# Optimization experiments

Hardware: AMD Instinct MI355X
Metric: run time of the kernel (lower is better)

Reference implementation:

```python
import jax, jax.numpy as jnp
import numpy as np

B, T, D = 1, 2048, 1024
HQ, HKV, HD = 16, 4, 64
G = HQ // HKV
E, TOPK, F = 8, 2, 2752
LB = 0.01
SCALE = HD ** -0.5


def setup_inputs() -> dict:
    key = jax.random.key(0)
    ks = jax.random.split(key, 12)
    s = 0.02
    return {
        "x": jax.random.normal(ks[0], (B, T, D), jnp.float32),
        "g1": jnp.ones((D,), jnp.float32),
        "g2": jnp.ones((D,), jnp.float32),
        "wq": jax.random.normal(ks[1], (D, HQ * HD), jnp.float32) * s,
        "wk": jax.random.normal(ks[2], (D, HKV * HD), jnp.float32) * s,
        "wv": jax.random.normal(ks[3], (D, HKV * HD), jnp.float32) * s,
        "wo": jax.random.normal(ks[4], (D, D), jnp.float32) * s,
        "gate_w": jax.random.normal(ks[5], (D, E), jnp.float32) * s,
        "we_gate": jax.random.normal(ks[6], (E, D, F), jnp.float32) * s,
        "we_up": jax.random.normal(ks[7], (E, D, F), jnp.float32) * s,
        "we_down": jax.random.normal(ks[8], (E, F, D), jnp.float32) * s,
    }


def _rmsnorm(x, g, eps=1e-6):
    return x * g * jax.lax.rsqrt(jnp.mean(x * x, axis=-1, keepdims=True) + eps)


def _rope(q, k):
    # q: [B,HQ,T,HD], k: [B,HKV,T,HD]; standard rotate-half RoPE
    pos = jnp.arange(T, dtype=jnp.float32)
    inv_freq = 1.0 / (10000.0 ** (jnp.arange(0, HD, 2, dtype=jnp.float32) / HD))
    ang = pos[:, None] * inv_freq[None, :]                  # [T, HD/2]
    cos = jnp.concatenate([jnp.cos(ang), jnp.cos(ang)], -1)  # [T, HD]
    sin = jnp.concatenate([jnp.sin(ang), jnp.sin(ang)], -1)

    def rot_half(x):
        x1, x2 = jnp.split(x, 2, axis=-1)
        return jnp.concatenate([-x2, x1], axis=-1)

    def apply(x):
        return x * cos + rot_half(x) * sin
    return apply(q), apply(k)


def _attention(x, g1, wq, wk, wv, wo):
    h = _rmsnorm(x, g1)
    q = (h @ wq).reshape(B, T, HQ, HD).transpose(0, 2, 1, 3)   # [B,HQ,T,HD]
    k = (h @ wk).reshape(B, T, HKV, HD).transpose(0, 2, 1, 3)  # [B,HKV,T,HD]
    v = (h @ wv).reshape(B, T, HKV, HD).transpose(0, 2, 1, 3)
    q, k = _rope(q, k)
    qg = q.reshape(B, HKV, G, T, HD)
    # grouped scores without materializing repeated K/V
    scores = jnp.einsum('bkgtd,bksd->bkgts', qg, k) * SCALE     # [B,HKV,G,T,T]
    causal = jnp.tril(jnp.ones((T, T), bool))
    scores = jnp.where(causal, scores, jnp.float32(-jnp.inf))
    w = jax.nn.softmax(scores, axis=-1)
    o = jnp.einsum('bkgts,bksd->bkgtd', w, v)                  # [B,HKV,G,T,HD]
    o = o.reshape(B, HQ, T, HD).transpose(0, 2, 1, 3).reshape(B, T, D)
    return o @ wo


def _moe(x, g2, gate_w, we_gate, we_up, we_down):
    h = _rmsnorm(x, g2).reshape(B * T, D)                      # [N,D]
    N = B * T
    logits = h @ gate_w                                        # [N,E]
    probs = jax.nn.softmax(logits, axis=-1)
    topv, topi = jax.lax.top_k(probs, TOPK)                    # [N,TOPK]
    topv = topv / (topv.sum(-1, keepdims=True) + 1e-8)
    # dense combine weights [N,E]: same math as masked per-expert dispatch
    combine = jnp.zeros((N, E), h.dtype).at[jnp.arange(N)[:, None], topi].add(topv)
    gh = jnp.einsum('nd,edf->enf', h, we_gate)
    up = jnp.einsum('nd,edf->enf', h, we_up)
    y = jnp.einsum('enf,efd->end', jax.nn.silu(gh) * up, we_down)
    out = jnp.einsum('end,ne->nd', y, combine).reshape(B, T, D)
    # load-balancing aux loss
    frac = jnp.zeros((E,), probs.dtype).at[topi.reshape(-1)].add(1.0) / (N * TOPK)
    load = probs.mean(axis=0)
    aux = LB * E * jnp.sum(frac * load)
    return out, aux


def reference(x, g1, g2, wq, wk, wv, wo, gate_w, we_gate, we_up, we_down):
    x = x + _attention(x, g1, wq, wk, wv, wo)
    moe_out, aux = _moe(x, g2, gate_w, we_gate, we_up, we_down)
    x = x + moe_out
    return x, aux
```

## Files before the change

### kernel.cpp

```cpp
#include <hip/hip_runtime.h>
#include <cstdint>

typedef __attribute__((ext_vector_type(8))) short short8;
typedef __attribute__((ext_vector_type(4))) float floatx4;
typedef __attribute__((ext_vector_type(4))) unsigned short ushort4v;
typedef unsigned short ushort;

#define T_LEN 2048
#define D_DIM 1024
#define HQn 16
#define HKVn 4
#define NE 8
#define FF 2752
#define NTOK 2048
#define NSLOT 4096
#define ATT_SCALE 0.125f
#define GATE_TPB 16

#define WAITCNT(N) asm volatile("s_waitcnt vmcnt(" #N ")" ::: "memory")

__device__ inline ushort f2bf(float f) {
  union { float f; unsigned int i; } v; v.f = f;
  unsigned int r = v.i + 0x7fffu + ((v.i >> 16) & 1u);
  return (ushort)(r >> 16);
}
__device__ inline float bf2f(ushort h) {
  union { unsigned int i; float f; } v; v.i = ((unsigned int)h) << 16;
  return v.f;
}
__device__ inline void split8(const float* v, short8& hi, short8& lo) {
#pragma unroll
  for (int i = 0; i < 8; i++) {
    ushort h = f2bf(v[i]);
    hi[i] = (short)h;
    lo[i] = (short)f2bf(v[i] - bf2f(h));
  }
}
__device__ inline floatx4 mfma16(short8 a, short8 b, floatx4 c) {
  return __builtin_amdgcn_mfma_f32_16x16x32_bf16(a, b, c, 0, 0, 0);
}
#define DMA16(g, l)                                                              \
  __builtin_amdgcn_global_load_lds((const __attribute__((address_space(1))) void*)(g), \
                                   (__attribute__((address_space(3))) void*)(l), 16, 0, 0)

__global__ __launch_bounds__(256) void k_cvtT(const float* __restrict__ src,
                                              ushort* __restrict__ dst, int R, int C) {
  __shared__ float tile[32][33];
  size_t sb = (size_t)blockIdx.z * R * C;
  const float* s = src + sb;
  ushort* d = dst + sb;
  int r0 = blockIdx.y * 32, c0 = blockIdx.x * 32;
  int tc = threadIdx.x & 31, tr = threadIdx.x >> 5;
#pragma unroll
  for (int i = 0; i < 4; i++)
    tile[tr + i * 8][tc] = s[(size_t)(r0 + tr + i * 8) * C + c0 + tc];
  __syncthreads();
#pragma unroll
  for (int i = 0; i < 4; i++) {
    int cc = tr + i * 8;
    d[(size_t)(c0 + cc) * R + r0 + tc] = f2bf(tile[tc][cc]);
  }
}

__global__ __launch_bounds__(256) void k_cvtT2(const float* __restrict__ src,
                                               ushort* __restrict__ dh,
                                               ushort* __restrict__ dl, int R, int C) {
  __shared__ float tile[32][33];
  int r0 = blockIdx.y * 32, c0 = blockIdx.x * 32;
  int tc = threadIdx.x & 31, tr = threadIdx.x >> 5;
#pragma unroll
  for (int i = 0; i < 4; i++)
    tile[tr + i * 8][tc] = src[(size_t)(r0 + tr + i * 8) * C + c0 + tc];
  __syncthreads();
#pragma unroll
  for (int i = 0; i < 4; i++) {
    int cc = tr + i * 8;
    float v = tile[tc][cc];
    ushort h = f2bf(v);
    dh[(size_t)(c0 + cc) * R + r0 + tc] = h;
    dl[(size_t)(c0 + cc) * R + r0 + tc] = f2bf(v - bf2f(h));
  }
}

__global__ __launch_bounds__(256) void k_rmsnorm2(const float* __restrict__ x,
                                                  const float* __restrict__ g,
                                                  ushort* __restrict__ oh,
                                                  ushort* __restrict__ ol) {
  int row = blockIdx.x;
  int t = threadIdx.x;
  const float4* x4 = (const float4*)(x + (size_t)row * D_DIM);
  float4 v = x4[t];
  float ss = v.x * v.x + v.y * v.y + v.z * v.z + v.w * v.w;
#pragma unroll
  for (int off = 32; off; off >>= 1) ss += __shfl_xor(ss, off, 64);
  __shared__ float red[4];
  if ((t & 63) == 0) red[t >> 6] = ss;
  __syncthreads();
  float tot = red[0] + red[1] + red[2] + red[3];
  float sc = rsqrtf(tot * (1.0f / D_DIM) + 1e-6f);
  const float4* g4 = (const float4*)g;
  float4 gv = g4[t];
  float vals[4] = {v.x * gv.x * sc, v.y * gv.y * sc, v.z * gv.z * sc, v.w * gv.w * sc};
  ushort4v h4, l4;
#pragma unroll
  for (int i = 0; i < 4; i++) {
    ushort h = f2bf(vals[i]);
    h4[i] = h;
    l4[i] = f2bf(vals[i] - bf2f(h));
  }
  *(ushort4v*)(oh + (size_t)row * D_DIM + t * 4) = h4;
  *(ushort4v*)(ol + (size_t)row * D_DIM + t * 4) = l4;
}

__global__ __launch_bounds__(256) void k_sgemm(const ushort* __restrict__ Ahg,
                                               const ushort* __restrict__ Alg,
                                               const ushort* __restrict__ Bhg,
                                               const ushort* __restrict__ Blg,
                                               float* __restrict__ C,
                                               const float* __restrict__ res,
                                               int N, int K) {
  __shared__ __align__(16) ushort L[36864];
  int tid = threadIdx.x;
  int m0 = blockIdx.y * 64, n0 = blockIdx.x * 128;
  int wave = tid >> 6, lane = tid & 63, quad = lane >> 4, l15 = lane & 15;
  int wm = (wave >> 1) * 32, wn = (wave & 1) * 64;
  floatx4 acc[2][4];
#pragma unroll
  for (int i = 0; i < 2; i++)
#pragma unroll
    for (int j = 0; j < 4; j++) acc[i][j] = (floatx4){0.f, 0.f, 0.f, 0.f};
  const ushort* src[6];
  int off[6];
  int srow = lane >> 2;
  int kc = ((lane & 3) ^ ((lane >> 3) & 3)) * 8;
#pragma unroll
  for (int j = 0; j < 6; j++) {
    int c = wave * 6 + j;
    if (c < 4) {
      src[j] = Ahg + (size_t)(m0 + c * 16 + srow) * K + kc;
      off[j] = c * 512;
    } else if (c < 8) {
      src[j] = Alg + (size_t)(m0 + (c - 4) * 16 + srow) * K + kc;
      off[j] = 2048 + (c - 4) * 512;
    } else if (c < 16) {
      src[j] = Bhg + (size_t)(n0 + (c - 8) * 16 + srow) * K + kc;
      off[j] = 4096 + (c - 8) * 512;
    } else {
      src[j] = Blg + (size_t)(n0 + (c - 16) * 16 + srow) * K + kc;
      off[j] = 8192 + (c - 16) * 512;
    }
  }
  auto stage = [&](ushort* Ld, int k0) {
#pragma unroll
    for (int j = 0; j < 6; j++) DMA16(src[j] + k0, Ld + off[j]);
  };
  auto compute = [&](const ushort* Ld) {
    const ushort* Ah = Ld;
    const ushort* Al = Ld + 2048;
    const ushort* Bh = Ld + 4096;
    const ushort* Bl = Ld + 8192;
    short8 ah[2], al[2], bh[4], bl[4];
#pragma unroll
    for (int mt = 0; mt < 2; mt++) {
      int ar = wm + mt * 16 + l15;
      int sw = (quad ^ ((ar >> 1) & 3)) * 8;
      ah[mt] = *(short8*)&Ah[ar * 32 + sw];
      al[mt] = *(short8*)&Al[ar * 32 + sw];
    }
#pragma unroll
    for (int nt = 0; nt < 4; nt++) {
      int br = wn + nt * 16 + l15;
      int sw = (quad ^ ((br >> 1) & 3)) * 8;
      bh[nt] = *(short8*)&Bh[br * 32 + sw];
      bl[nt] = *(short8*)&Bl[br * 32 + sw];
    }
#pragma unroll
    for (int mt = 0; mt < 2; mt++)
#pragma unroll
      for (int nt = 0; nt < 4; nt++) {
        acc[mt][nt] = mfma16(ah[mt], bh[nt], acc[mt][nt]);
        acc[mt][nt] = mfma16(ah[mt], bl[nt], acc[mt][nt]);
        acc[mt][nt] = mfma16(al[mt], bh[nt], acc[mt][nt]);
      }
  };
  int ntile = K >> 5;
  stage(L, 0);
  stage(L + 12288, 32);
  int cb = 0;
  for (int t = 0; t < ntile; t++) {
    if (t + 1 < ntile) { WAITCNT(6); } else { WAITCNT(0); }
    __builtin_amdgcn_s_barrier();
    __builtin_amdgcn_sched_barrier(0);
    if (t + 2 < ntile) {
      int sb = cb + 2; if (sb >= 3) sb -= 3;
      stage(L + sb * 12288, (t + 2) << 5);
    }
    compute(L + cb * 12288);
    if (++cb == 3) cb = 0;
  }
#pragma unroll
  for (int mt = 0; mt < 2; mt++) {
    int row = m0 + wm + mt * 16 + quad * 4;
#pragma unroll
    for (int nt2 = 0; nt2 < 4; nt2++) {
      int col = n0 + wn + nt2 * 16 + l15;
#pragma unroll
      for (int r = 0; r < 4; r++) {
        float v = acc[mt][nt2][r];
        if (res) v += res[(size_t)(row + r) * N + col];
        C[(size_t)(row + r) * N + col] = v;
      }
    }
  }
}

__global__ __launch_bounds__(256) void k_rope_cvt(const float* __restrict__ qkvf,
                                                  ushort* __restrict__ qhi,
                                                  ushort* __restrict__ qlo,
                                                  ushort* __restrict__ khi,
                                                  ushort* __restrict__ klo) {
  int t = blockIdx.x;
  const float* row = qkvf + (size_t)t * 1536;
  for (int it = threadIdx.x; it < (HQn + HKVn) * 32; it += 256) {
    int hh = it >> 5, i = it & 31;
    float inv = powf(10000.0f, -(float)i / 32.0f);
    float ang = (float)t * inv;
    float c = cosf(ang), s = sinf(ang);
    const float* p;
    ushort *dh, *dl;
    size_t base;
    if (hh < HQn) {
      p = row + hh * 64;
      base = ((size_t)hh * T_LEN + t) * 64;
      dh = qhi; dl = qlo;
    } else {
      int h2 = hh - HQn;
      p = row + 1024 + h2 * 64;
      base = ((size_t)h2 * T_LEN + t) * 64;
      dh = khi; dl = klo;
    }
    float a = p[i], b = p[i + 32];
    float v0 = a * c - b * s;
    float v1 = b * c + a * s;
    ushort h0 = f2bf(v0);
    dh[base + i] = h0;
    dl[base + i] = f2bf(v0 - bf2f(h0));
    ushort h1 = f2bf(v1);
    dh[base + i + 32] = h1;
    dl[base + i + 32] = f2bf(v1 - bf2f(h1));
  }
}

__global__ __launch_bounds__(256) void k_vT(const float* __restrict__ qkvf,
                                            ushort* __restrict__ vbth,
                                            ushort* __restrict__ vbtl) {
  __shared__ float tile[32][33];
  int t0 = blockIdx.x * 32;
  int dh = blockIdx.y;
  int col0 = 1280 + dh * 32;
  int tc = threadIdx.x & 31, tr = threadIdx.x >> 5;
#pragma unroll
  for (int i = 0; i < 4; i++)
    tile[tr + i * 8][tc] = qkvf[(size_t)(t0 + tr + i * 8) * 1536 + col0 + tc];
  __syncthreads();
#pragma unroll
  for (int i = 0; i < 4; i++) {
    int dd = tr + i * 8;
    float v = tile[tc][dd];
    ushort h = f2bf(v);
    size_t idx = (size_t)(dh * 32 + dd) * T_LEN + t0 + tc;
    vbth[idx] = h;
    vbtl[idx] = f2bf(v - bf2f(h));
  }
}

__global__ __launch_bounds__(256) void k_attn(const ushort* __restrict__ qhi,
                                              const ushort* __restrict__ qlo,
                                              const ushort* __restrict__ khi,
                                              const ushort* __restrict__ klo,
                                              const ushort* __restrict__ vbth,
                                              const ushort* __restrict__ vbtl,
                                              ushort* __restrict__ obh,
                                              ushort* __restrict__ obl) {
  __shared__ __align__(16) ushort Kh[4096], Kl[4096], Vh[4096], Vl[4096];
  __shared__ ushort Psh[4 * 16 * 72], Psl[4 * 16 * 72];
  int qh = blockIdx.y, kvh = qh >> 2;
  int tid = threadIdx.x, wave = tid >> 6, lane = tid & 63;
  int quad = lane >> 4, l15 = lane & 15;
  int sx = l15 >> 1;
  int rlb = lane >> 3;
  int csb = (lane & 7) ^ (lane >> 4);
#pragma unroll 1
  for (int hf = 0; hf < 2; hf++) {
    int xt = hf ? (31 - (int)blockIdx.x) : (int)blockIdx.x;
    int r0 = xt * 64;
    const ushort* qbh_ = qhi + ((size_t)qh * T_LEN + r0 + wave * 16 + l15) * 64;
    const ushort* qbl_ = qlo + ((size_t)qh * T_LEN + r0 + wave * 16 + l15) * 64;
    short8 aqh0 = *(const short8*)&qbh_[quad * 8];
    short8 aqh1 = *(const short8*)&qbh_[32 + quad * 8];
    short8 aql0 = *(const short8*)&qbl_[quad * 8];
    short8 aql1 = *(const short8*)&qbl_[32 + quad * 8];
    floatx4 oacc[4];
#pragma unroll
    for (int nt = 0; nt < 4; nt++) oacc[nt] = (floatx4){0.f, 0.f, 0.f, 0.f};
    float mrun[4], lrun[4];
#pragma unroll
    for (int r = 0; r < 4; r++) { mrun[r] = -INFINITY; lrun[r] = 0.f; }
    for (int cc = 0; cc <= xt; cc++) {
      __syncthreads();
      if (wave < 2) {
        const ushort* G = (wave == 0) ? khi : klo;
        ushort* L = (wave == 0) ? Kh : Kl;
        size_t rbase = (size_t)kvh * T_LEN + cc * 64;
#pragma unroll
        for (int i = 0; i < 8; i++) {
          int ch = csb ^ ((i & 1) * 4);
          DMA16(G + (rbase + i * 8 + rlb) * 64 + ch * 8, L + i * 512);
        }
      } else {
        const ushort* G = (wave == 2) ? vbth : vbtl;
        ushort* L = (wave == 2) ? Vh : Vl;
#pragma unroll
        for (int i = 0; i < 8; i++) {
          int ch = csb ^ ((i & 1) * 4);
          DMA16(G + ((size_t)(kvh * 64 + i * 8 + rlb)) * T_LEN + cc * 64 + ch * 8,
                L + i * 512);
        }
      }
      __syncthreads();
      floatx4 s[4];
#pragma unroll
      for (int nt = 0; nt < 4; nt++) {
        int row = nt * 16 + l15;
        short8 bh0 = *(short8*)&Kh[row * 64 + (quad ^ sx) * 8];
        short8 bh1 = *(short8*)&Kh[row * 64 + ((4 + quad) ^ sx) * 8];
        short8 bl0 = *(short8*)&Kl[row * 64 + (quad ^ sx) * 8];
        short8 bl1 = *(short8*)&Kl[row * 64 + ((4 + quad) ^ sx) * 8];
        floatx4 z = (floatx4){0.f, 0.f, 0.f, 0.f};
        z = mfma16(aqh0, bh0, z);
        z = mfma16(aqh1, bh1, z);
        z = mfma16(aqh0, bl0, z);
        z = mfma16(aqh1, bl1, z);
        z = mfma16(aql0, bh0, z);
        z = mfma16(aql1, bh1, z);
        s[nt] = z;
      }
      int rowg0 = r0 + wave * 16 + quad * 4;
#pragma unroll
      for (int nt = 0; nt < 4; nt++) {
        int colg = cc * 64 + nt * 16 + l15;
#pragma unroll
        for (int r = 0; r < 4; r++) {
          float v = s[nt][r] * ATT_SCALE;
          s[nt][r] = (colg > rowg0 + r) ? -INFINITY : v;
        }
      }
      float mnew[4], alpha[4], psum[4];
#pragma unroll
      for (int r = 0; r < 4; r++) {
        float mx = fmaxf(fmaxf(s[0][r], s[1][r]), fmaxf(s[2][r], s[3][r]));
#pragma unroll
        for (int off = 1; off < 16; off <<= 1) mx = fmaxf(mx, __shfl_xor(mx, off, 64));
        mnew[r] = fmaxf(mrun[r], mx);
        psum[r] = 0.f;
      }
#pragma unroll
      for (int nt = 0; nt < 4; nt++)
#pragma unroll
        for (int r = 0; r < 4; r++) {
          float p = __expf(s[nt][r] - mnew[r]);
          s[nt][r] = p;
          psum[r] += p;
        }
#pragma unroll
      for (int r = 0; r < 4; r++) {
        float ps = psum[r];
#pragma unroll
        for (int off = 1; off < 16; off <<= 1) ps += __shfl_xor(ps, off, 64);
        alpha[r] = __expf(mrun[r] - mnew[r]);
        lrun[r] = lrun[r] * alpha[r] + ps;
        mrun[r] = mnew[r];
      }
#pragma unroll
      for (int nt = 0; nt < 4; nt++)
#pragma unroll
        for (int r = 0; r < 4; r++) oacc[nt][r] *= alpha[r];
#pragma unroll
      for (int nt = 0; nt < 4; nt++)
#pragma unroll
        for (int r = 0; r < 4; r++) {
          float p = s[nt][r];
          ushort ph = f2bf(p);
          Psh[wave * 1152 + (quad * 4 + r) * 72 + nt * 16 + l15] = ph;
          Psl[wave * 1152 + (quad * 4 + r) * 72 + nt * 16 + l15] = f2bf(p - bf2f(ph));
        }
      short8 aph0 = *(short8*)&Psh[wave * 1152 + l15 * 72 + quad * 8];
      short8 aph1 = *(short8*)&Psh[wave * 1152 + l15 * 72 + 32 + quad * 8];
      short8 apl0 = *(short8*)&Psl[wave * 1152 + l15 * 72 + quad * 8];
      short8 apl1 = *(short8*)&Psl[wave * 1152 + l15 * 72 + 32 + quad * 8];
#pragma unroll
      for (int nt = 0; nt < 4; nt++) {
        int row = nt * 16 + l15;
        short8 bvh0 = *(short8*)&Vh[row * 64 + (quad ^ sx) * 8];
        short8 bvh1 = *(short8*)&Vh[row * 64 + ((4 + quad) ^ sx) * 8];
        short8 bvl0 = *(short8*)&Vl[row * 64 + (quad ^ sx) * 8];
        short8 bvl1 = *(short8*)&Vl[row * 64 + ((4 + quad) ^ sx) * 8];
        oacc[nt] = mfma16(aph0, bvh0, oacc[nt]);
        oacc[nt] = mfma16(aph1, bvh1, oacc[nt]);
        oacc[nt] = mfma16(aph0, bvl0, oacc[nt]);
        oacc[nt] = mfma16(aph1, bvl1, oacc[nt]);
        oacc[nt] = mfma16(apl0, bvh0, oacc[nt]);
        oacc[nt] = mfma16(apl1, bvh1, oacc[nt]);
      }
    }
#pragma unroll
    for (int nt = 0; nt < 4; nt++)
#pragma unroll
      for (int r = 0; r < 4; r++) {
        int rowg = r0 + wave * 16 + quad * 4 + r;
        float v = oacc[nt][r] / lrun[r];
        ushort h = f2bf(v);
        size_t idx = (size_t)rowg * D_DIM + qh * 64 + nt * 16 + l15;
        obh[idx] = h;
        obl[idx] = f2bf(v - bf2f(h));
      }
  }
}

__global__ __launch_bounds__(256) void k_gate(const float* __restrict__ x1,
                                              const float* __restrict__ g2,
                                              const float* __restrict__ gw,
                                              int* __restrict__ counts,
                                              int* __restrict__ ids,
                                              float* __restrict__ wts,
                                              float* __restrict__ load_sum) {
  __shared__ float lsum[NE];
  __shared__ int lcount[NE];
  __shared__ int lbase[NE];
  __shared__ int ltok[GATE_TPB * 2];
  __shared__ int lexp[GATE_TPB * 2];
  __shared__ float lwt[GATE_TPB * 2];
  int tid = threadIdx.x, wave = tid >> 6, lane = tid & 63;
  if (tid < NE) { lsum[tid] = 0.f; lcount[tid] = 0; }
  __syncthreads();
  int t0 = blockIdx.x * GATE_TPB;
#pragma unroll
  for (int tt = 0; tt < GATE_TPB / 4; tt++) {
    int tloc = tt * 4 + wave;
    int token = t0 + tloc;
    const float* xp = x1 + (size_t)token * D_DIM;
    float acc[NE] = {};
    float ss = 0.f;
    for (int d = lane; d < D_DIM; d += 64) {
      float xv = xp[d];
      ss += xv * xv;
      float hv = xv * g2[d];
#pragma unroll
      for (int e = 0; e < NE; e++) acc[e] += hv * gw[d * NE + e];
    }
#pragma unroll
    for (int off = 32; off; off >>= 1) ss += __shfl_xor(ss, off, 64);
#pragma unroll
    for (int e = 0; e < NE; e++)
#pragma unroll
      for (int off = 32; off; off >>= 1) acc[e] += __shfl_xor(acc[e], off, 64);
    if (lane == 0) {
      float sc = rsqrtf(ss * (1.0f / D_DIM) + 1e-6f);
      float mx = -1e30f;
#pragma unroll
      for (int e = 0; e < NE; e++) { acc[e] *= sc; mx = fmaxf(mx, acc[e]); }
      float p[NE], sum = 0.f;
#pragma unroll
      for (int e = 0; e < NE; e++) { p[e] = expf(acc[e] - mx); sum += p[e]; }
#pragma unroll
      for (int e = 0; e < NE; e++) p[e] /= sum;
      int i1 = 0;
#pragma unroll
      for (int e = 1; e < NE; e++) if (acc[e] > acc[i1]) i1 = e;
      int i2 = (i1 == 0) ? 1 : 0;
#pragma unroll
      for (int e = 0; e < NE; e++) if (e != i1 && acc[e] > acc[i2]) i2 = e;
      float denom = p[i1] + p[i2] + 1e-8f;
      int slot = tloc * 2;
      lexp[slot] = i1; ltok[slot] = token; lwt[slot] = p[i1] / denom;
      lexp[slot + 1] = i2; ltok[slot + 1] = token; lwt[slot + 1] = p[i2] / denom;
      atomicAdd(&lcount[i1], 1);
      atomicAdd(&lcount[i2], 1);
#pragma unroll
      for (int e = 0; e < NE; e++) atomicAdd(&lsum[e], p[e]);
    }
  }
  __syncthreads();
  if (tid < NE) {
    lbase[tid] = atomicAdd(&counts[tid], lcount[tid]);
    atomicAdd(&load_sum[tid], lsum[tid]);
    lcount[tid] = 0;
  }
  __syncthreads();
  if (tid < GATE_TPB * 2) {
    int e = lexp[tid];
    int off = atomicAdd(&lcount[e], 1);
    int pos = lbase[e] + off;
    ids[e * NTOK + pos] = ltok[tid];
    wts[e * NTOK + pos] = lwt[tid];
  }
}

__global__ void k_offsets(const int* __restrict__ counts, int* __restrict__ offsets) {
  if (threadIdx.x == 0 && blockIdx.x == 0) {
    int s = 0;
    for (int e = 0; e < NE; e++) { offsets[e] = s; s += counts[e]; }
  }
}

__global__ __launch_bounds__(256) void k_moe_gateup(const ushort* __restrict__ h,
                                                    const ushort* __restrict__ wgT,
                                                    const ushort* __restrict__ wuT,
                                                    const int* __restrict__ ids,
                                                    const float* __restrict__ wts,
                                                    const int* __restrict__ counts,
                                                    const int* __restrict__ offsets,
                                                    ushort* __restrict__ act) {
  int p = blockIdx.x;
  int k8 = p & 7, q = p >> 3;
  int G = (q >> 4) * 8 + k8;
  int m = q & 15;
  int e = G / 43;
  int n = G - e * 43;
  int cnt = counts[e];
  int m0 = m * 128;
  if (m0 >= cnt) return;
  int n0 = n * 64;
  __shared__ __align__(16) ushort L0[8192], L1[8192];
  __shared__ int toks[128];
  __shared__ float wrow[128];
  int tid = threadIdx.x;
  if (tid < 128) {
    int mm = m0 + tid;
    toks[tid] = (mm < cnt) ? ids[e * NTOK + mm] : 0;
    wrow[tid] = (mm < cnt) ? wts[e * NTOK + mm] : 0.f;
  }
  __syncthreads();
  int wave = tid >> 6, lane = tid & 63, quad = lane >> 4, l15 = lane & 15;
  int wm = (wave >> 1) * 64, wn = (wave & 1) * 32;
  const ushort* Wg = wgT + (size_t)e * FF * D_DIM;
  const ushort* Wu = wuT + (size_t)e * FF * D_DIM;
  const ushort* src[4];
  int off[4];
  int srow = lane >> 2;
  int kc = ((lane & 3) ^ ((lane >> 3) & 3)) * 8;
#pragma unroll
  for (int j = 0; j < 4; j++) {
    int c = wave * 4 + j;
    if (c < 8) {
      src[j] = h + (size_t)toks[c * 16 + srow] * D_DIM + kc;
      off[j] = c * 512;
    } else if (c < 12) {
      src[j] = Wg + (size_t)(n0 + (c - 8) * 16 + srow) * D_DIM + kc;
      off[j] = 4096 + (c - 8) * 512;
    } else {
      src[j] = Wu + (size_t)(n0 + (c - 12) * 16 + srow) * D_DIM + kc;
      off[j] = 6144 + (c - 12) * 512;
    }
  }
  floatx4 accg[4][2], accu[4][2];
#pragma unroll
  for (int i = 0; i < 4; i++)
#pragma unroll
    for (int j = 0; j < 2; j++) {
      accg[i][j] = (floatx4){0.f, 0.f, 0.f, 0.f};
      accu[i][j] = (floatx4){0.f, 0.f, 0.f, 0.f};
    }
  auto stage = [&](ushort* Ld, int k0) {
#pragma unroll
    for (int j = 0; j < 4; j++) DMA16(src[j] + k0, Ld + off[j]);
  };
  auto compute = [&](const ushort* Ld) {
    const ushort* As = Ld;
    const ushort* Bg = Ld + 4096;
    const ushort* Bu = Ld + 6144;
    short8 aF[4], bgF[2], buF[2];
#pragma unroll
    for (int mt = 0; mt < 4; mt++) {
      int ar = wm + mt * 16 + l15;
      int sw = (quad ^ ((ar >> 1) & 3)) * 8;
      aF[mt] = *(short8*)&As[ar * 32 + sw];
    }
#pragma unroll
    for (int nt = 0; nt < 2; nt++) {
      int br = wn + nt * 16 + l15;
      int sw = (quad ^ ((br >> 1) & 3)) * 8;
      bgF[nt] = *(short8*)&Bg[br * 32 + sw];
      buF[nt] = *(short8*)&Bu[br * 32 + sw];
    }
#pragma unroll
    for (int mt = 0; mt < 4; mt++)
#pragma unroll
      for (int nt = 0; nt < 2; nt++) {
        accg[mt][nt] = mfma16(aF[mt], bgF[nt], accg[mt][nt]);
        accu[mt][nt] = mfma16(aF[mt], buF[nt], accu[mt][nt]);
      }
  };
  stage(L0, 0);
  __syncthreads();
  for (int t = 0; t < 32; t++) {
    if ((t & 1) == 0) {
      if (t + 1 < 32) stage(L1, (t + 1) << 5);
      compute(L0);
    } else {
      if (t + 1 < 32) stage(L0, (t + 1) << 5);
      compute(L1);
    }
    __syncthreads();
  }
  int aoff = offsets[e];
#pragma unroll
  for (int mt = 0; mt < 4; mt++) {
    int mrow = wm + mt * 16 + quad * 4;
#pragma unroll
    for (int nt = 0; nt < 2; nt++) {
      int col = n0 + wn + nt * 16 + l15;
#pragma unroll
      for (int r = 0; r < 4; r++) {
        int ml = mrow + r;
        if (m0 + ml < cnt) {
          float g = accg[mt][nt][r];
          float u = accu[mt][nt][r];
          float sil = g / (1.f + __expf(-g));
          act[(size_t)(aoff + m0 + ml) * FF + col] = f2bf(sil * u * wrow[ml]);
        }
      }
    }
  }
}

__global__ __launch_bounds__(256) void k_moe_down(const ushort* __restrict__ act,
                                                  const ushort* __restrict__ wdT,
                                                  const int* __restrict__ ids,
                                                  const int* __restrict__ counts,
                                                  const int* __restrict__ offsets,
                                                  float* __restrict__ moe_acc) {
  int p = blockIdx.x;
  int k8 = p & 7, q = p >> 3;
  int G = (q >> 4) * 8 + k8;
  int m = q & 15;
  int z = G >> 3;
  int n = G & 7;
  int e = z & 7, kh = z >> 3;
  int cnt = counts[e];
  int m0 = m * 128;
  if (m0 >= cnt) return;
  int n0 = n * 128;
  __shared__ __align__(16) ushort L[24576];
  __shared__ int toks[128];
  int tid = threadIdx.x;
  if (tid < 128) {
    int mm = m0 + tid;
    toks[tid] = (mm < cnt) ? ids[e * NTOK + mm] : 0;
  }
  __syncthreads();
  int wave = tid >> 6, lane = tid & 63, quad = lane >> 4, l15 = lane & 15;
  int wm = (wave >> 1) * 64, wn = (wave & 1) * 64;
  int aoff = offsets[e];
  const ushort* Wd = wdT + (size_t)e * D_DIM * FF;
  const ushort* src[4];
  int off[4];
  int srow = lane >> 2;
  int kc = ((lane & 3) ^ ((lane >> 3) & 3)) * 8;
#pragma unroll
  for (int j = 0; j < 4; j++) {
    int c = wave * 4 + j;
    if (c < 8) {
      src[j] = act + (size_t)(aoff + m0 + c * 16 + srow) * FF + kc;
      off[j] = c * 512;
    } else {
      src[j] = Wd + (size_t)(n0 + (c - 8) * 16 + srow) * FF + kc;
      off[j] = 4096 + (c - 8) * 512;
    }
  }
  floatx4 acc[4][4];
#pragma unroll
  for (int i = 0; i < 4; i++)
#pragma unroll
    for (int j = 0; j < 4; j++) acc[i][j] = (floatx4){0.f, 0.f, 0.f, 0.f};
  auto stage = [&](ushort* Ld, int k0) {
#pragma unroll
    for (int j = 0; j < 4; j++) DMA16(src[j] + k0, Ld + off[j]);
  };
  auto compute = [&](const ushort* Ld) {
    const ushort* As = Ld;
    const ushort* Bs = Ld + 4096;
    short8 aF[4], bF[4];
#pragma unroll
    for (int mt = 0; mt < 4; mt++) {
      int ar = wm + mt * 16 + l15;
      int sw = (quad ^ ((ar >> 1) & 3)) * 8;
      aF[mt] = *(short8*)&As[ar * 32 + sw];
    }
#pragma unroll
    for (int nt = 0; nt < 4; nt++) {
      int br = wn + nt * 16 + l15;
      int sw = (quad ^ ((br >> 1) & 3)) * 8;
      bF[nt] = *(short8*)&Bs[br * 32 + sw];
    }
#pragma unroll
    for (int mt = 0; mt < 4; mt++)
#pragma unroll
      for (int nt = 0; nt < 4; nt++) acc[mt][nt] = mfma16(aF[mt], bF[nt], acc[mt][nt]);
  };
  int kbeg = kh * 1376;
  stage(L, kbeg);
  stage(L + 8192, kbeg + 32);
  int cb = 0;
  for (int t = 0; t < 43; t++) {
    if (t + 1 < 43) { WAITCNT(4); } else { WAITCNT(0); }
    __builtin_amdgcn_s_barrier();
    __builtin_amdgcn_sched_barrier(0);
    if (t + 2 < 43) {
      int sb = cb + 2; if (sb >= 3) sb -= 3;
      stage(L + sb * 8192, kbeg + ((t + 2) << 5));
    }
    compute(L + cb * 8192);
    if (++cb == 3) cb = 0;
  }
#pragma unroll
  for (int mt = 0; mt < 4; mt++) {
    int mrow = wm + mt * 16 + quad * 4;
#pragma unroll
    for (int nt2 = 0; nt2 < 4; nt2++) {
      int col = n0 + wn + nt2 * 16 + l15;
#pragma unroll
      for (int r = 0; r < 4; r++) {
        int ml = mrow + r;
        if (m0 + ml < cnt)
          atomicAdd(&moe_acc[(size_t)toks[ml] * D_DIM + col], acc[mt][nt2][r]);
      }
    }
  }
}

__global__ __launch_bounds__(256) void k_add(const float* __restrict__ a,
                                             const float* __restrict__ b,
                                             float* __restrict__ o) {
  int i = blockIdx.x * 256 + threadIdx.x;
  float4 va = ((const float4*)a)[i];
  float4 vb = ((const float4*)b)[i];
  float4 vo;
  vo.x = va.x + vb.x; vo.y = va.y + vb.y; vo.z = va.z + vb.z; vo.w = va.w + vb.w;
  ((float4*)o)[i] = vo;
}

__global__ void k_aux(const int* __restrict__ counts, const float* __restrict__ load_sum,
                      float* __restrict__ out_aux) {
  if (threadIdx.x == 0 && blockIdx.x == 0) {
    float s = 0.f;
    for (int e = 0; e < NE; e++)
      s += ((float)counts[e] / (float)NSLOT) * (load_sum[e] / (float)NTOK);
    *out_aux = 0.01f * (float)NE * s;
  }
}

extern "C" void kernel_launch(void* const* d_in, const int* in_sizes, int n_in,
                              void* d_out, int out_size, void* d_ws, size_t ws_size,
                              hipStream_t stream) {
  const float* x = (const float*)d_in[0];
  const float* g1 = (const float*)d_in[1];
  const float* g2 = (const float*)d_in[2];
  const float* wq = (const float*)d_in[3];
  const float* wk = (const float*)d_in[4];
  const float* wv = (const float*)d_in[5];
  const float* wo = (const float*)d_in[6];
  const float* gate_w = (const float*)d_in[7];
  const float* we_gate = (const float*)d_in[8];
  const float* we_up = (const float*)d_in[9];
  const float* we_down = (const float*)d_in[10];
  float* out = (float*)d_out;

  char* w = (char*)d_ws;
  size_t o = 0;
  auto alloc = [&](size_t bytes) -> char* {
    char* p = w + o;
    o = (o + bytes + 255) & ~(size_t)255;
    return p;
  };
  ushort* h1h = (ushort*)alloc((size_t)NTOK * D_DIM * 2);
  ushort* h1l = (ushort*)alloc((size_t)NTOK * D_DIM * 2);
  float* qkvf = (float*)alloc((size_t)NTOK * 1536 * 4);
  ushort* qhi = (ushort*)alloc((size_t)HQn * T_LEN * 64 * 2);
  ushort* qlo = (ushort*)alloc((size_t)HQn * T_LEN * 64 * 2);
  ushort* khi = (ushort*)alloc((size_t)HKVn * T_LEN * 64 * 2);
  ushort* klo = (ushort*)alloc((size_t)HKVn * T_LEN * 64 * 2);
  ushort* vbth = (ushort*)alloc((size_t)HKVn * 64 * T_LEN * 2);
  ushort* vbtl = (ushort*)alloc((size_t)HKVn * 64 * T_LEN * 2);
  ushort* obh = (ushort*)alloc((size_t)NTOK * D_DIM * 2);
  ushort* obl = (ushort*)alloc((size_t)NTOK * D_DIM * 2);
  float* x1 = (float*)alloc((size_t)NTOK * D_DIM * 4);
  float* moe_acc = (float*)alloc((size_t)NTOK * D_DIM * 4);
  ushort* act = (ushort*)alloc((size_t)(NSLOT + 128) * FF * 2);
  ushort* qkvwTh = (ushort*)alloc((size_t)1536 * 1024 * 2);
  ushort* qkvwTl = (ushort*)alloc((size_t)1536 * 1024 * 2);
  ushort* woTh = (ushort*)alloc((size_t)1024 * 1024 * 2);
  ushort* woTl = (ushort*)alloc((size_t)1024 * 1024 * 2);
  ushort* h2h = (ushort*)alloc((size_t)NTOK * D_DIM * 2);
  ushort* h2l = (ushort*)alloc((size_t)NTOK * D_DIM * 2);
  ushort* wgT = (ushort*)alloc((size_t)NE * FF * D_DIM * 2);
  ushort* wuT = (ushort*)alloc((size_t)NE * FF * D_DIM * 2);
  ushort* wdT = (ushort*)alloc((size_t)NE * D_DIM * FF * 2);
  int* counts = (int*)alloc(NE * 4);
  int* offsets = (int*)alloc(NE * 4);
  float* load_sum = (float*)alloc(NE * 4);
  int* ids = (int*)alloc((size_t)NE * NTOK * 4);
  float* wts = (float*)alloc((size_t)NE * NTOK * 4);

  hipMemsetAsync(moe_acc, 0, (size_t)NTOK * D_DIM * 4, stream);
  hipMemsetAsync(counts, 0, 768, stream);

  k_cvtT2<<<dim3(32, 32), 256, 0, stream>>>(wq, qkvwTh, qkvwTl, 1024, 1024);
  k_cvtT2<<<dim3(8, 32), 256, 0, stream>>>(wk, qkvwTh + (size_t)1024 * 1024,
                                           qkvwTl + (size_t)1024 * 1024, 1024, 256);
  k_cvtT2<<<dim3(8, 32), 256, 0, stream>>>(wv, qkvwTh + (size_t)1280 * 1024,
                                           qkvwTl + (size_t)1280 * 1024, 1024, 256);
  k_cvtT2<<<dim3(32, 32), 256, 0, stream>>>(wo, woTh, woTl, 1024, 1024);
  k_cvtT<<<dim3(86, 32, 8), 256, 0, stream>>>(we_gate, wgT, 1024, 2752);
  k_cvtT<<<dim3(86, 32, 8), 256, 0, stream>>>(we_up, wuT, 1024, 2752);
  k_cvtT<<<dim3(32, 86, 8), 256, 0, stream>>>(we_down, wdT, 2752, 1024);

  k_rmsnorm2<<<NTOK, 256, 0, stream>>>(x, g1, h1h, h1l);
  k_sgemm<<<dim3(12, 32), 256, 0, stream>>>(h1h, h1l, qkvwTh, qkvwTl, qkvf, nullptr,
                                            1536, 1024);
  k_rope_cvt<<<T_LEN, 256, 0, stream>>>(qkvf, qhi, qlo, khi, klo);
  k_vT<<<dim3(64, 8), 256, 0, stream>>>(qkvf, vbth, vbtl);
  k_attn<<<dim3(16, 16), 256, 0, stream>>>(qhi, qlo, khi, klo, vbth, vbtl, obh, obl);
  k_sgemm<<<dim3(8, 32), 256, 0, stream>>>(obh, obl, woTh, woTl, x1, x, 1024, 1024);

  k_rmsnorm2<<<NTOK, 256, 0, stream>>>(x1, g2, h2h, h2l);
  k_gate<<<NTOK / GATE_TPB, 256, 0, stream>>>(x1, g2, gate_w, counts, ids, wts, load_sum);
  k_offsets<<<1, 1, 0, stream>>>(counts, offsets);
  k_moe_gateup<<<5504, 256, 0, stream>>>(h2h, wgT, wuT, ids, wts, counts, offsets, act);
  k_moe_down<<<2048, 256, 0, stream>>>(act, wdT, ids, counts, offsets, moe_acc);
  k_add<<<(NTOK * D_DIM) / (256 * 4), 256, 0, stream>>>(x1, moe_acc, out);
  k_aux<<<1, 1, 0, stream>>>(counts, load_sum, out + (size_t)NTOK * D_DIM);
}
```

Before: 675.7 us.

## Double K-tile depth in MoE gate/up GEMM and stage router weights in LDS

The MoE gate/up kernel now stages K=64 per iteration instead of 32. That halves the loop trip count and barriers, and issues twice as many async loads per stage, with the LDS swizzle changed to an 8-chunk XOR pattern. Separately, the router kernel copies the gate weight matrix into shared memory in transposed form before the dot products, so global reads are coalesced instead of strided. LDS use per gate/up block doubles (64KB for the buffers), which may lower occupancy. The router now pays a 32KB load per block in exchange.

```diff
diff --git a/kernel.cpp b/kernel.cpp
--- a/kernel.cpp
+++ b/kernel.cpp
@@ -434,6 +434,7 @@
                                               int* __restrict__ ids,
                                               float* __restrict__ wts,
                                               float* __restrict__ load_sum) {
+  __shared__ float gwT[NE][D_DIM];
   __shared__ float lsum[NE];
   __shared__ int lcount[NE];
   __shared__ int lbase[NE];
@@ -441,6 +442,10 @@
   __shared__ int lexp[GATE_TPB * 2];
   __shared__ float lwt[GATE_TPB * 2];
   int tid = threadIdx.x, wave = tid >> 6, lane = tid & 63;
+  for (int i = tid; i < NE * D_DIM; i += 256) {
+    int d = i >> 3, e2 = i & 7;
+    gwT[e2][d] = gw[i];
+  }
   if (tid < NE) { lsum[tid] = 0.f; lcount[tid] = 0; }
   __syncthreads();
   int t0 = blockIdx.x * GATE_TPB;
@@ -456,7 +461,7 @@
       ss += xv * xv;
       float hv = xv * g2[d];
 #pragma unroll
-      for (int e = 0; e < NE; e++) acc[e] += hv * gw[d * NE + e];
+      for (int e = 0; e < NE; e++) acc[e] += hv * gwT[e][d];
     }
 #pragma unroll
     for (int off = 32; off; off >>= 1) ss += __shfl_xor(ss, off, 64);
@@ -531,7 +536,7 @@
   int m0 = m * 128;
   if (m0 >= cnt) return;
   int n0 = n * 64;
-  __shared__ __align__(16) ushort L0[8192], L1[8192];
+  __shared__ __align__(16) ushort L0[16384], L1[16384];
   __shared__ int toks[128];
   __shared__ float wrow[128];
   int tid = threadIdx.x;
@@ -545,22 +550,22 @@
   int wm = (wave >> 1) * 64, wn = (wave & 1) * 32;
   const ushort* Wg = wgT + (size_t)e * FF * D_DIM;
   const ushort* Wu = wuT + (size_t)e * FF * D_DIM;
-  const ushort* src[4];
-  int off[4];
-  int srow = lane >> 2;
-  int kc = ((lane & 3) ^ ((lane >> 3) & 3)) * 8;
-#pragma unroll
-  for (int j = 0; j < 4; j++) {
-    int c = wave * 4 + j;
-    if (c < 8) {
-      src[j] = h + (size_t)toks[c * 16 + srow] * D_DIM + kc;
+  const ushort* src[8];
+  int off[8];
+  int srow = lane >> 3;
+  int kc = ((lane & 7) ^ ((lane >> 3) & 7)) * 8;
+#pragma unroll
+  for (int j = 0; j < 8; j++) {
+    int c = wave * 8 + j;
+    if (c < 16) {
+      src[j] = h + (size_t)toks[c * 8 + srow] * D_DIM + kc;
       off[j] = c * 512;
-    } else if (c < 12) {
-      src[j] = Wg + (size_t)(n0 + (c - 8) * 16 + srow) * D_DIM + kc;
-      off[j] = 4096 + (c - 8) * 512;
+    } else if (c < 24) {
+      src[j] = Wg + (size_t)(n0 + (c - 16) * 8 + srow) * D_DIM + kc;
+      off[j] = 8192 + (c - 16) * 512;
     } else {
-      src[j] = Wu + (size_t)(n0 + (c - 12) * 16 + srow) * D_DIM + kc;
-      off[j] = 6144 + (c - 12) * 512;
+      src[j] = Wu + (size_t)(n0 + (c - 24) * 8 + srow) * D_DIM + kc;
+      off[j] = 12288 + (c - 24) * 512;
     }
   }
   floatx4 accg[4][2], accu[4][2];
@@ -573,42 +578,50 @@
     }
   auto stage = [&](ushort* Ld, int k0) {
 #pragma unroll
-    for (int j = 0; j < 4; j++) DMA16(src[j] + k0, Ld + off[j]);
+    for (int j = 0; j < 8; j++) DMA16(src[j] + k0, Ld + off[j]);
   };
   auto compute = [&](const ushort* Ld) {
     const ushort* As = Ld;
-    const ushort* Bg = Ld + 4096;
-    const ushort* Bu = Ld + 6144;
-    short8 aF[4], bgF[2], buF[2];
+    const ushort* Bg = Ld + 8192;
+    const ushort* Bu = Ld + 12288;
+    short8 aF[4][2], bgF[2][2], buF[2][2];
 #pragma unroll
     for (int mt = 0; mt < 4; mt++) {
       int ar = wm + mt * 16 + l15;
-      int sw = (quad ^ ((ar >> 1) & 3)) * 8;
-      aF[mt] = *(short8*)&As[ar * 32 + sw];
+#pragma unroll
+      for (int hh = 0; hh < 2; hh++) {
+        int ch = (quad + hh * 4) ^ (ar & 7);
+        aF[mt][hh] = *(short8*)&As[ar * 64 + ch * 8];
+      }
     }
 #pragma unroll
     for (int nt = 0; nt < 2; nt++) {
       int br = wn + nt * 16 + l15;
-      int sw = (quad ^ ((br >> 1) & 3)) * 8;
-      bgF[nt] = *(short8*)&Bg[br * 32 + sw];
-      buF[nt] = *(short8*)&Bu[br * 32 + sw];
+#pragma unroll
+      for (int hh = 0; hh < 2; hh++) {
+        int ch = (quad + hh * 4) ^ (br & 7);
+        bgF[nt][hh] = *(short8*)&Bg[br * 64 + ch * 8];
+        buF[nt][hh] = *(short8*)&Bu[br * 64 + ch * 8];
+      }
     }
 #pragma unroll
     for (int mt = 0; mt < 4; mt++)
 #pragma unroll
       for (int nt = 0; nt < 2; nt++) {
-        accg[mt][nt] = mfma16(aF[mt], bgF[nt], accg[mt][nt]);
-        accu[mt][nt] = mfma16(aF[mt], buF[nt], accu[mt][nt]);
+        accg[mt][nt] = mfma16(aF[mt][0], bgF[nt][0], accg[mt][nt]);
+        accg[mt][nt] = mfma16(aF[mt][1], bgF[nt][1], accg[mt][nt]);
+        accu[mt][nt] = mfma16(aF[mt][0], buF[nt][0], accu[mt][nt]);
+        accu[mt][nt] = mfma16(aF[mt][1], buF[nt][1], accu[mt][nt]);
       }
   };
   stage(L0, 0);
   __syncthreads();
-  for (int t = 0; t < 32; t++) {
+  for (int t = 0; t < 16; t++) {
     if ((t & 1) == 0) {
-      if (t + 1 < 32) stage(L1, (t + 1) << 5);
+      if (t + 1 < 16) stage(L1, (t + 1) << 6);
       compute(L0);
     } else {
-      if (t + 1 < 32) stage(L0, (t + 1) << 5);
+      if (t + 1 < 16) stage(L0, (t + 1) << 6);
       compute(L1);
     }
     __syncthreads();
```

Result: no change. 688.2 us (+1.8%).
